# Kernel tuning notes

Hardware: AMD Instinct MI355X
Metric: run time of the kernel (lower is better)

Reference implementation:

```python
import jax, jax.numpy as jnp
import numpy as np
import math

D_MODEL = 1024
MAX_SEQ_LEN = 2048
BATCH = 4
SEQ_LEN = 2048

def setup_inputs() -> dict:
    key = jax.random.key(0)
    kx, kq, kk, kv = jax.random.split(key, 4)
    x = jax.random.normal(kx, (BATCH, SEQ_LEN, D_MODEL), dtype=jnp.float32)
    # nn.Linear(d_model, d_model, bias=False): weight shape [out, in]; y = x @ W.T
    s = 1.0 / math.sqrt(D_MODEL)
    wq = jax.random.uniform(kq, (D_MODEL, D_MODEL), dtype=jnp.float32, minval=-s, maxval=s)
    wk = jax.random.uniform(kk, (D_MODEL, D_MODEL), dtype=jnp.float32, minval=-s, maxval=s)
    wv = jax.random.uniform(kv, (D_MODEL, D_MODEL), dtype=jnp.float32, minval=-s, maxval=s)
    return {"x": x, "wq": wq, "wk": wk, "wv": wv}

def reference(x, wq, wk, wv):
    # q,k,v: [B, S, D]
    q = jnp.einsum('bsd,ed->bse', x, wq)
    k = jnp.einsum('bsd,ed->bse', x, wk)
    v = jnp.einsum('bsd,ed->bse', x, wv)
    scale = 1.0 / math.sqrt(q.shape[-1])
    scores = jnp.einsum('bqd,bkd->bqk', q, k) * scale  # [B, S, S]
    seq_len = x.shape[1]
    causal = jnp.tril(jnp.ones((seq_len, seq_len), dtype=bool))
    scores = jnp.where(causal[None, :, :], scores, -jnp.inf)
    attn = jax.nn.softmax(scores, axis=-1)
    return jnp.einsum('bqk,bkd->bqd', attn, v)
```

## Files before the change

### kernel.cpp

```cpp
#include <hip/hip_runtime.h>
#include <hip/hip_bf16.h>

typedef unsigned short u16;
typedef __attribute__((ext_vector_type(8))) short short8;
typedef __attribute__((ext_vector_type(4))) float f32x4;

__device__ __forceinline__ u16 f2bf(float f){
  unsigned int u = __builtin_bit_cast(unsigned int, f);
  u += 0x7FFFu + ((u >> 16) & 1u);
  return (u16)(u >> 16);
}
__device__ __forceinline__ float bf2f(u16 b){
  unsigned int u = ((unsigned int)b) << 16;
  return __builtin_bit_cast(float, u);
}

__device__ __forceinline__ void gload_lds16(const u16* g, u16* lds){
  __builtin_amdgcn_global_load_lds(
      (const __attribute__((address_space(1))) unsigned int*)g,
      (__attribute__((address_space(3))) unsigned int*)lds, 16, 0, 0);
}

template<int MODE>
__launch_bounds__(256, 4)
__global__ void gemm_bt(const u16* __restrict__ A, int lda,
                        const u16* __restrict__ B, int ldb,
                        void* __restrict__ Cout, int ldc,
                        int kIterFixed,
                        long long strideAz, long long strideBz, long long strideCz,
                        float* __restrict__ lsum, float scale)
{
  __shared__ __align__(16) u16 As[2][128*32];
  __shared__ __align__(16) u16 Bs[2][128*32];
  int bi, bj, bz;
  if (MODE == 2){
    const int d = blockIdx.x;
    const int r = d & 255;
    bi = (d >> 8) ? (15 - (r & 7)) : (r & 7);
    bj = (r >> 3) & 7;
    bz = r >> 6;
  } else {
    bi = blockIdx.x; bj = blockIdx.y; bz = blockIdx.z;
    if (MODE == 1 && bj > bi) return;
  }
  A += (long long)bz * strideAz;
  B += (long long)bz * strideBz;
  const int m0 = bi*128, n0 = bj*128;
  const int kIters = (MODE == 2) ? (bi + 1) * 4 : kIterFixed;
  const int t = threadIdx.x;
  const int lane = t & 63;
  const int w = t >> 6;
  const int wm = w >> 1, wn = w & 1;
  const int la = lane & 15, lb = lane >> 4;

  const int r0 = t >> 2,          q0c = (t & 3) << 3;
  const int r1 = (t + 256) >> 2,  q1c = (t & 3) << 3;
  const int ldsb0 = (t & ~63) << 3;
  const int ldsb1 = (256 + (t & ~63)) << 3;

  f32x4 acc[4][4];
  #pragma unroll
  for (int i = 0; i < 4; i++)
    #pragma unroll
    for (int j = 0; j < 4; j++) acc[i][j] = (f32x4){0.f, 0.f, 0.f, 0.f};

  gload_lds16(A + (long long)(m0 + r0)*lda + q0c, &As[0][ldsb0]);
  gload_lds16(A + (long long)(m0 + r1)*lda + q1c, &As[0][ldsb1]);
  gload_lds16(B + (long long)(n0 + r0)*ldb + q0c, &Bs[0][ldsb0]);
  gload_lds16(B + (long long)(n0 + r1)*ldb + q1c, &Bs[0][ldsb1]);
  asm volatile("s_waitcnt vmcnt(0)" ::: "memory");
  __syncthreads();

  for (int kt = 0; kt < kIters; ++kt){
    const int cur = kt & 1;
    if (kt + 1 < kIters){
      const int k0 = (kt + 1) * 32;
      gload_lds16(A + (long long)(m0 + r0)*lda + k0 + q0c, &As[cur^1][ldsb0]);
      gload_lds16(A + (long long)(m0 + r1)*lda + k0 + q1c, &As[cur^1][ldsb1]);
      gload_lds16(B + (long long)(n0 + r0)*ldb + k0 + q0c, &Bs[cur^1][ldsb0]);
      gload_lds16(B + (long long)(n0 + r1)*ldb + k0 + q1c, &Bs[cur^1][ldsb1]);
    }
    short8 af[4], bfr[4];
    #pragma unroll
    for (int mi = 0; mi < 4; mi++)
      af[mi] = *(const short8*)&As[cur][(wm*64 + mi*16 + la)*32 + lb*8];
    #pragma unroll
    for (int ni = 0; ni < 4; ni++)
      bfr[ni] = *(const short8*)&Bs[cur][(wn*64 + ni*16 + la)*32 + lb*8];
    #pragma unroll
    for (int mi = 0; mi < 4; mi++)
      #pragma unroll
      for (int ni = 0; ni < 4; ni++)
        acc[mi][ni] = __builtin_amdgcn_mfma_f32_16x16x32_bf16(af[mi], bfr[ni], acc[mi][ni], 0, 0, 0);
    asm volatile("s_waitcnt vmcnt(0)" ::: "memory");
    __syncthreads();
  }

  if (MODE == 0){
    u16* C = (u16*)Cout;
    #pragma unroll
    for (int mi = 0; mi < 4; mi++)
      #pragma unroll
      for (int r = 0; r < 4; r++){
        const int row = m0 + wm*64 + mi*16 + lb*4 + r;
        #pragma unroll
        for (int ni = 0; ni < 4; ni++){
          const int col = n0 + wn*64 + ni*16 + la;
          C[(long long)row*ldc + col] = f2bf(acc[mi][ni][r]);
        }
      }
  } else if (MODE == 1){
    u16* C = (u16*)Cout + (long long)bz * strideCz;
    float* lrow = lsum + bz*2048;
    #pragma unroll
    for (int mi = 0; mi < 4; mi++)
      #pragma unroll
      for (int r = 0; r < 4; r++){
        const int row = m0 + wm*64 + mi*16 + lb*4 + r;
        float partial = 0.f;
        #pragma unroll
        for (int ni = 0; ni < 4; ni++){
          const int col = n0 + wn*64 + ni*16 + la;
          float p = 0.f;
          if (col <= row) p = __expf(acc[mi][ni][r] * scale);
          const u16 ub = f2bf(p);
          C[(long long)row*ldc + col] = ub;
          partial += bf2f(ub);
        }
        #pragma unroll
        for (int off = 1; off < 16; off <<= 1) partial += __shfl_xor(partial, off);
        if (la == 0) atomicAdd(&lrow[row], partial);
      }
  } else {
    float* C = (float*)Cout + (long long)bz * strideCz;
    const float* lrow = lsum + bz*2048;
    #pragma unroll
    for (int mi = 0; mi < 4; mi++)
      #pragma unroll
      for (int r = 0; r < 4; r++){
        const int row = m0 + wm*64 + mi*16 + lb*4 + r;
        const float inv = 1.f / lrow[row];
        #pragma unroll
        for (int ni = 0; ni < 4; ni++){
          const int col = n0 + wn*64 + ni*16 + la;
          C[(long long)row*ldc + col] = acc[mi][ni][r] * inv;
        }
      }
  }
}

__global__ void convert_bf16(const float* __restrict__ src, u16* __restrict__ dst, int n4){
  const int i = blockIdx.x*256 + threadIdx.x;
  if (i >= n4) return;
  const float4 v = ((const float4*)src)[i];
  union { u16 u[4]; unsigned long long ll; } o;
  o.u[0] = f2bf(v.x); o.u[1] = f2bf(v.y); o.u[2] = f2bf(v.z); o.u[3] = f2bf(v.w);
  ((unsigned long long*)dst)[i] = o.ll;
}

__global__ void transpose_v(const u16* __restrict__ qkvb, u16* __restrict__ vt){
  __shared__ u16 tile[32][33];
  const int b = blockIdx.z;
  const int s0 = blockIdx.x*32, d0 = blockIdx.y*32;
  const int tx = threadIdx.x, ty = threadIdx.y;
  const u16* src = qkvb + (long long)b*2048*3072 + 2048;
  #pragma unroll
  for (int i = 0; i < 4; i++){
    const int s = ty + i*8;
    tile[s][tx] = src[(long long)(s0 + s)*3072 + d0 + tx];
  }
  __syncthreads();
  u16* dst = vt + (long long)b*1024*2048;
  #pragma unroll
  for (int i = 0; i < 4; i++){
    const int d = ty + i*8;
    dst[(long long)(d0 + d)*2048 + s0 + tx] = tile[tx][d];
  }
}

extern "C" void kernel_launch(void* const* d_in, const int* in_sizes, int n_in,
                              void* d_out, int out_size, void* d_ws, size_t ws_size,
                              hipStream_t stream)
{
  const float* x  = (const float*)d_in[0];
  const float* wq = (const float*)d_in[1];
  const float* wk = (const float*)d_in[2];
  const float* wv = (const float*)d_in[3];

  u16* xb   = (u16*)d_ws;
  u16* wb   = xb   + (size_t)8192*1024;
  u16* qkvb = wb   + (size_t)3072*1024;
  u16* vt   = qkvb + (size_t)8192*3072;
  u16* Pb   = vt   + (size_t)4*1024*2048;
  float* lsum = (float*)(Pb + (size_t)4*2048*2048);

  convert_bf16<<<8192, 256, 0, stream>>>(x,  xb, 2097152);
  convert_bf16<<<1024, 256, 0, stream>>>(wq, wb,                     262144);
  convert_bf16<<<1024, 256, 0, stream>>>(wk, wb + (size_t)1024*1024, 262144);
  convert_bf16<<<1024, 256, 0, stream>>>(wv, wb + (size_t)2048*1024, 262144);

  gemm_bt<0><<<dim3(64, 24, 1), 256, 0, stream>>>(
      xb, 1024, wb, 1024, (void*)qkvb, 3072, 32, 0, 0, 0, nullptr, 1.f);

  transpose_v<<<dim3(64, 32, 4), dim3(32, 8, 1), 0, stream>>>(qkvb, vt);

  hipMemsetAsync(lsum, 0, (size_t)4*2048*sizeof(float), stream);

  gemm_bt<1><<<dim3(16, 16, 4), 256, 0, stream>>>(
      qkvb, 3072, qkvb + 1024, 3072, (void*)Pb, 2048, 32,
      (long long)2048*3072, (long long)2048*3072, (long long)2048*2048,
      lsum, 0.03125f);

  gemm_bt<2><<<dim3(512, 1, 1), 256, 0, stream>>>(
      Pb, 2048, vt, 2048, d_out, 1024, 0,
      (long long)2048*2048, (long long)1024*2048, (long long)2048*1024,
      lsum, 1.f);
}
```

Baseline: 259.9 us.

## Add 256x256-tile 8-wave pipelined GEMM for QKV projection and scores

```diff
diff --git a/kernel.cpp b/kernel.cpp
--- a/kernel.cpp
+++ b/kernel.cpp
@@ -14,11 +14,159 @@
   unsigned int u = ((unsigned int)b) << 16;
   return __builtin_bit_cast(float, u);
 }
-
 __device__ __forceinline__ void gload_lds16(const u16* g, u16* lds){
   __builtin_amdgcn_global_load_lds(
       (const __attribute__((address_space(1))) unsigned int*)g,
       (__attribute__((address_space(3))) unsigned int*)lds, 16, 0, 0);
+}
+
+#define FENCE_LGKM0() do { asm volatile("s_waitcnt lgkmcnt(0)" ::: "memory"); \
+                           __builtin_amdgcn_sched_barrier(0); } while(0)
+#define FENCE_VMN(N)  do { asm volatile("s_waitcnt vmcnt(" #N ")" ::: "memory"); \
+                           __builtin_amdgcn_sched_barrier(0); } while(0)
+
+__device__ __forceinline__ void stage_half(const u16* p, u16* arr, int bufhalf, int dstOff){
+  u16* d = arr + bufhalf*8192 + dstOff;
+  gload_lds16(p, d);
+  gload_lds16(p + 32, d + 4096);
+}
+
+template<int MODE>
+__launch_bounds__(512, 2)
+__global__ void gemm8p(const u16* __restrict__ A, int lda,
+                       const u16* __restrict__ B, int ldb,
+                       void* __restrict__ Cout, int ldc,
+                       long long strideAz, long long strideBz, long long strideCz,
+                       float* __restrict__ lsum, float scale)
+{
+  __shared__ __align__(16) u16 As[32768];
+  __shared__ __align__(16) u16 Bs[32768];
+  constexpr int NS = 16;
+
+  int bi, bj, bz;
+  if (MODE == 0){
+    const int bid = blockIdx.x;
+    const int swz = (bid & 7)*48 + (bid >> 3);
+    bi = swz & 31; bj = swz >> 5; bz = 0;
+  } else {
+    bi = blockIdx.x; bj = blockIdx.y; bz = blockIdx.z;
+    if (bj > bi) return;
+  }
+  A += (long long)bz * strideAz;
+  B += (long long)bz * strideBz;
+  const int m0 = bi*256, n0 = bj*256;
+
+  const int t = threadIdx.x;
+  const int lane = t & 63;
+  const int w = t >> 6;
+  const int wm = w >> 2, wn = w & 3;
+  const int la = lane & 15, lb = lane >> 4;
+
+  const int srow = (t >> 2) & 127;
+  const int scol = ((t & 3) ^ (((t >> 5) & 1) << 1)) * 8;
+  const u16* pA0 = A + (long long)(m0 +       srow)*lda + scol;
+  const u16* pA1 = A + (long long)(m0 + 128 + srow)*lda + scol;
+  const u16* pB0 = B + (long long)(n0 +       srow)*ldb + scol;
+  const u16* pB1 = B + (long long)(n0 + 128 + srow)*ldb + scol;
+  const int dstOff = (t & ~63) * 8;
+
+  const int colr = (lb*8) ^ ((la & 8) << 1);
+
+  f32x4 acc[8][4];
+  #pragma unroll
+  for (int m = 0; m < 8; ++m)
+    #pragma unroll
+    for (int n = 0; n < 4; ++n) acc[m][n] = (f32x4){0.f,0.f,0.f,0.f};
+
+  stage_half(pB0,      Bs, 0, dstOff);
+  stage_half(pB1,      Bs, 1, dstOff);
+  stage_half(pA0,      As, 0, dstOff);
+  stage_half(pA1,      As, 1, dstOff);
+  stage_half(pB0 + 64, Bs, 2, dstOff);
+  stage_half(pB1 + 64, Bs, 3, dstOff);
+  FENCE_VMN(4);
+  __builtin_amdgcn_s_barrier();
+
+  for (int s = 0; s < NS; ++s){
+    const int buf = s & 1;
+    const int Ab = (buf*2 + wm) * 8192;
+    const int Bb = (buf*2 + (wn >> 1)) * 8192;
+    short8 bfr[4][2];
+    #pragma unroll
+    for (int q = 0; q < 4; ++q){
+      short8 af[2][2];
+      #pragma unroll
+      for (int mm = 0; mm < 2; ++mm)
+        #pragma unroll
+        for (int kk = 0; kk < 2; ++kk)
+          af[mm][kk] = *(const short8*)&As[Ab + kk*4096 + ((2*q+mm)*16 + la)*32 + colr];
+      if (q == 0){
+        #pragma unroll
+        for (int n = 0; n < 4; ++n)
+          #pragma unroll
+          for (int kk = 0; kk < 2; ++kk)
+            bfr[n][kk] = *(const short8*)&Bs[Bb + kk*4096 + ((wn&1)*64 + n*16 + la)*32 + colr];
+      }
+      if (q == 0 && s+1 < NS) stage_half(pA0 + (s+1)*64, As, ((s+1)&1)*2 + 0, dstOff);
+      if (q == 1 && s+1 < NS) stage_half(pA1 + (s+1)*64, As, ((s+1)&1)*2 + 1, dstOff);
+      if (q == 2 && s+2 < NS) stage_half(pB0 + (s+2)*64, Bs, buf*2 + 0, dstOff);
+      if (q == 3 && s+2 < NS) stage_half(pB1 + (s+2)*64, Bs, buf*2 + 1, dstOff);
+
+      __builtin_amdgcn_s_barrier();
+      FENCE_LGKM0();
+      __builtin_amdgcn_s_setprio(1);
+      #pragma unroll
+      for (int mm = 0; mm < 2; ++mm)
+        #pragma unroll
+        for (int n = 0; n < 4; ++n)
+          #pragma unroll
+          for (int kk = 0; kk < 2; ++kk)
+            acc[2*q+mm][n] = __builtin_amdgcn_mfma_f32_16x16x32_bf16(
+                                af[mm][kk], bfr[n][kk], acc[2*q+mm][n], 0,0,0);
+      __builtin_amdgcn_s_setprio(0);
+      if (q == 3 && s+1 < NS){
+        if (s+2 < NS) { FENCE_VMN(4); } else { FENCE_VMN(0); }
+      }
+      __builtin_amdgcn_s_barrier();
+    }
+  }
+
+  if (MODE == 0){
+    u16* C = (u16*)Cout;
+    #pragma unroll
+    for (int m = 0; m < 8; ++m)
+      #pragma unroll
+      for (int r = 0; r < 4; ++r){
+        const int row = m0 + wm*128 + m*16 + lb*4 + r;
+        #pragma unroll
+        for (int n = 0; n < 4; ++n){
+          const int col = n0 + wn*64 + n*16 + la;
+          C[(long long)row*ldc + col] = f2bf(acc[m][n][r]);
+        }
+      }
+  } else {
+    u16* C = (u16*)Cout + (long long)bz * strideCz;
+    float* lrow = lsum + bz*2048;
+    #pragma unroll
+    for (int m = 0; m < 8; ++m)
+      #pragma unroll
+      for (int r = 0; r < 4; ++r){
+        const int row = m0 + wm*128 + m*16 + lb*4 + r;
+        float partial = 0.f;
+        #pragma unroll
+        for (int n = 0; n < 4; ++n){
+          const int col = n0 + wn*64 + n*16 + la;
+          float p = 0.f;
+          if (col <= row) p = __expf(acc[m][n][r] * scale);
+          const u16 ub = f2bf(p);
+          C[(long long)row*ldc + col] = ub;
+          partial += bf2f(ub);
+        }
+        #pragma unroll
+        for (int off = 1; off < 16; off <<= 1) partial += __shfl_xor(partial, off);
+        if (la == 0) atomicAdd(&lrow[row], partial);
+      }
+  }
 }
 
 template<int MODE>
@@ -41,7 +189,6 @@
     bz = r >> 6;
   } else {
     bi = blockIdx.x; bj = blockIdx.y; bz = blockIdx.z;
-    if (MODE == 1 && bj > bi) return;
   }
   A += (long long)bz * strideAz;
   B += (long long)bz * strideBz;
@@ -96,42 +243,7 @@
     __syncthreads();
   }
 
-  if (MODE == 0){
-    u16* C = (u16*)Cout;
-    #pragma unroll
-    for (int mi = 0; mi < 4; mi++)
-      #pragma unroll
-      for (int r = 0; r < 4; r++){
-        const int row = m0 + wm*64 + mi*16 + lb*4 + r;
-        #pragma unroll
-        for (int ni = 0; ni < 4; ni++){
-          const int col = n0 + wn*64 + ni*16 + la;
-          C[(long long)row*ldc + col] = f2bf(acc[mi][ni][r]);
-        }
-      }
-  } else if (MODE == 1){
-    u16* C = (u16*)Cout + (long long)bz * strideCz;
-    float* lrow = lsum + bz*2048;
-    #pragma unroll
-    for (int mi = 0; mi < 4; mi++)
-      #pragma unroll
-      for (int r = 0; r < 4; r++){
-        const int row = m0 + wm*64 + mi*16 + lb*4 + r;
-        float partial = 0.f;
-        #pragma unroll
-        for (int ni = 0; ni < 4; ni++){
-          const int col = n0 + wn*64 + ni*16 + la;
-          float p = 0.f;
-          if (col <= row) p = __expf(acc[mi][ni][r] * scale);
-          const u16 ub = f2bf(p);
-          C[(long long)row*ldc + col] = ub;
-          partial += bf2f(ub);
-        }
-        #pragma unroll
-        for (int off = 1; off < 16; off <<= 1) partial += __shfl_xor(partial, off);
-        if (la == 0) atomicAdd(&lrow[row], partial);
-      }
-  } else {
+  {
     float* C = (float*)Cout + (long long)bz * strideCz;
     const float* lrow = lsum + bz*2048;
     #pragma unroll
@@ -199,15 +311,15 @@
   convert_bf16<<<1024, 256, 0, stream>>>(wk, wb + (size_t)1024*1024, 262144);
   convert_bf16<<<1024, 256, 0, stream>>>(wv, wb + (size_t)2048*1024, 262144);
 
-  gemm_bt<0><<<dim3(64, 24, 1), 256, 0, stream>>>(
-      xb, 1024, wb, 1024, (void*)qkvb, 3072, 32, 0, 0, 0, nullptr, 1.f);
+  gemm8p<0><<<dim3(384, 1, 1), 512, 0, stream>>>(
+      xb, 1024, wb, 1024, (void*)qkvb, 3072, 0, 0, 0, nullptr, 1.f);
 
   transpose_v<<<dim3(64, 32, 4), dim3(32, 8, 1), 0, stream>>>(qkvb, vt);
 
   hipMemsetAsync(lsum, 0, (size_t)4*2048*sizeof(float), stream);
 
-  gemm_bt<1><<<dim3(16, 16, 4), 256, 0, stream>>>(
-      qkvb, 3072, qkvb + 1024, 3072, (void*)Pb, 2048, 32,
+  gemm8p<1><<<dim3(8, 8, 4), 512, 0, stream>>>(
+      qkvb, 3072, qkvb + 1024, 3072, (void*)Pb, 2048,
       (long long)2048*3072, (long long)2048*3072, (long long)2048*2048,
       lsum, 0.03125f);
 
```

Result: no change. 259.9 us (-0.0%).
